# Performance work log

Measured on AMD Instinct MI355X. Metric: run time of the kernel, lower is better.

Reference implementation:

```python
import jax, jax.numpy as jnp
import numpy as np

WS = 11
SIGMA = 1.5
CH = 3
C1 = (0.01 * 255.0) ** 2  # 6.5025
C2 = (0.03 * 255.0) ** 2  # 58.5225


def _gauss_window():
    # 1D Gaussian -> outer product -> depthwise kernel [C, 1, ws, ws] (OIHW)
    coords = jnp.arange(WS, dtype=jnp.float32) - WS // 2
    g = jnp.exp(-coords ** 2 / (2.0 * SIGMA ** 2))
    g = g / g.sum()
    w2d = g[:, None] * g[None, :]
    return jnp.tile(w2d[None, None], (CH, 1, 1, 1))


def _dwconv(x, win):
    pad = WS // 2
    return jax.lax.conv_general_dilated(
        x, win, window_strides=(1, 1), padding=[(pad, pad), (pad, pad)],
        feature_group_count=CH,
        dimension_numbers=('NCHW', 'OIHW', 'NCHW'))


def setup_inputs() -> dict:
    key = jax.random.key(0)
    k1, k2 = jax.random.split(key)
    shape = (32, 3, 512, 512)
    img_gen = jax.random.uniform(k1, shape, jnp.float32, -1.0, 1.0)
    img_ref = jax.random.uniform(k2, shape, jnp.float32, -1.0, 1.0)
    return {"img_gen": img_gen, "img_ref": img_ref}


def reference(img_gen, img_ref):
    gen = (img_gen + 1.0) * 0.5
    ref = (img_ref + 1.0) * 0.5
    win = _gauss_window()

    mu1 = _dwconv(gen, win)
    mu2 = _dwconv(ref, win)
    mu1_sq = mu1 * mu1
    mu2_sq = mu2 * mu2
    mu1_mu2 = mu1 * mu2
    sigma1_sq = _dwconv(gen * gen, win) - mu1_sq
    sigma2_sq = _dwconv(ref * ref, win) - mu2_sq
    sigma12 = _dwconv(gen * ref, win) - mu1_mu2

    ssim_map = ((2.0 * mu1_mu2 + C1) * (2.0 * sigma12 + C2)) / (
        (mu1_sq + mu2_sq + C1) * (sigma1_sq + sigma2_sq + C2))
    return 1.0 - ssim_map.mean()
```

## Files before the change

kernel.cpp:

```cpp
#include <hip/hip_runtime.h>

#define TX 64
#define TY 20
#define PROWS (TY + 10)
#define HSTR 67
#define IMW 512
#define IMH 512
#define NPLANES 96
#define NBX (IMW / TX)
#define NBY ((IMH + TY - 1) / TY)
#define NBLOCKS (NBX * NBY * NPLANES)

__device__ __forceinline__ float uniform_f(float v) {
  return __int_as_float(__builtin_amdgcn_readfirstlane(__float_as_int(v)));
}

__device__ __forceinline__ void gauss_weights(float* w) {
  double t[11];
  double s = 0.0;
#pragma unroll
  for (int i = 0; i < 11; ++i) {
    double d = (double)(i - 5);
    t[i] = exp(-d * d / 4.5);
    s += t[i];
  }
#pragma unroll
  for (int i = 0; i < 11; ++i) w[i] = uniform_f((float)(t[i] / s));
}

__global__ __launch_bounds__(256, 4) void ssim_main(
    const float* __restrict__ gen, const float* __restrict__ ref,
    float* __restrict__ partial) {
  __shared__ float sh[5][PROWS][HSTR];
  __shared__ float swsum[4];

  const int tid = threadIdx.x;
  const int bid = blockIdx.x;
  const int rem = bid % (NBX * NBY);
  const int plane = bid / (NBX * NBY);
  const int bx = rem % NBX;
  const int by = rem / NBX;
  const int x0 = bx * TX;
  const int y0 = by * TY;
  const float* gp = gen + (size_t)plane * (IMW * IMH);
  const float* rp = ref + (size_t)plane * (IMW * IMH);

  float w[11];
  gauss_weights(w);

  if (tid < PROWS * 8) {
    const int row = tid >> 3;
    const int xs = (tid & 7) * 8;
    const int gy = y0 - 5 + row;
    const bool rowok = (gy >= 0) && (gy < IMH);
    const int xbase = x0 + xs - 8;
    const float* grow = gp + (size_t)gy * IMW;
    const float* rrow = rp + (size_t)gy * IMW;

    float ga[24], ra[24];
#pragma unroll
    for (int k = 0; k < 6; ++k) {
      const int c = xbase + 4 * k;
      const bool ok = rowok && (c >= 0) && (c < IMW);
      float4 vg = make_float4(0.f, 0.f, 0.f, 0.f);
      float4 vr = make_float4(0.f, 0.f, 0.f, 0.f);
      if (ok) {
        float4 g4 = *(const float4*)(grow + c);
        float4 r4 = *(const float4*)(rrow + c);
        vg.x = fmaf(0.5f, g4.x, 0.5f); vg.y = fmaf(0.5f, g4.y, 0.5f);
        vg.z = fmaf(0.5f, g4.z, 0.5f); vg.w = fmaf(0.5f, g4.w, 0.5f);
        vr.x = fmaf(0.5f, r4.x, 0.5f); vr.y = fmaf(0.5f, r4.y, 0.5f);
        vr.z = fmaf(0.5f, r4.z, 0.5f); vr.w = fmaf(0.5f, r4.w, 0.5f);
      }
      ga[4 * k + 0] = vg.x; ga[4 * k + 1] = vg.y;
      ga[4 * k + 2] = vg.z; ga[4 * k + 3] = vg.w;
      ra[4 * k + 0] = vr.x; ra[4 * k + 1] = vr.y;
      ra[4 * k + 2] = vr.z; ra[4 * k + 3] = vr.w;
    }

    float acc[5][8];
#pragma unroll
    for (int q = 0; q < 5; ++q)
#pragma unroll
      for (int o = 0; o < 8; ++o) acc[q][o] = 0.f;

#pragma unroll
    for (int p = 0; p < 18; ++p) {
      const float g = ga[p + 3];
      const float r = ra[p + 3];
      const float gg = g * g;
      const float rr = r * r;
      const float gr = g * r;
      const int olo = (p - 10 < 0) ? 0 : p - 10;
      const int ohi = (p < 7) ? p : 7;
#pragma unroll
      for (int o = olo; o <= ohi; ++o) {
        const float wt = w[p - o];
        acc[0][o] = fmaf(wt, g, acc[0][o]);
        acc[1][o] = fmaf(wt, r, acc[1][o]);
        acc[2][o] = fmaf(wt, gg, acc[2][o]);
        acc[3][o] = fmaf(wt, rr, acc[3][o]);
        acc[4][o] = fmaf(wt, gr, acc[4][o]);
      }
    }
#pragma unroll
    for (int q = 0; q < 5; ++q)
#pragma unroll
      for (int o = 0; o < 8; ++o) sh[q][row][xs + o] = acc[q][o];
  }
  __syncthreads();

  const int col = tid & 63;
  const int r0 = (tid >> 6) * 5;
  float hv[5][15];
#pragma unroll
  for (int q = 0; q < 5; ++q)
#pragma unroll
    for (int i = 0; i < 15; ++i) hv[q][i] = sh[q][r0 + i][col];

  const float C1 = 6.5025f, C2 = 58.5225f;
  float lsum = 0.f;
#pragma unroll
  for (int o = 0; o < 5; ++o) {
    float mu1 = 0.f, mu2 = 0.f, e1 = 0.f, e2 = 0.f, e12 = 0.f;
#pragma unroll
    for (int t = 0; t < 11; ++t) {
      const float wt = w[t];
      mu1 = fmaf(wt, hv[0][o + t], mu1);
      mu2 = fmaf(wt, hv[1][o + t], mu2);
      e1 = fmaf(wt, hv[2][o + t], e1);
      e2 = fmaf(wt, hv[3][o + t], e2);
      e12 = fmaf(wt, hv[4][o + t], e12);
    }
    const float m12 = mu1 * mu2;
    const float m1s = mu1 * mu1;
    const float m2s = mu2 * mu2;
    const float num = (2.f * m12 + C1) * (2.f * (e12 - m12) + C2);
    const float den = (m1s + m2s + C1) * ((e1 - m1s) + (e2 - m2s) + C2);
    const int y = y0 + r0 + o;
    lsum += (y < IMH) ? (num / den) : 0.f;
  }

#pragma unroll
  for (int off = 32; off > 0; off >>= 1) lsum += __shfl_down(lsum, off, 64);
  if ((tid & 63) == 0) swsum[tid >> 6] = lsum;
  __syncthreads();
  if (tid == 0) partial[bid] = swsum[0] + swsum[1] + swsum[2] + swsum[3];
}

__global__ void ssim_reduce(const float* __restrict__ partial,
                            float* __restrict__ out) {
  const int nv = NBLOCKS / 4;
  double s = 0.0;
  for (int i = threadIdx.x; i < nv; i += 256) {
    float4 v = ((const float4*)partial)[i];
    s += (double)v.x + (double)v.y + (double)v.z + (double)v.w;
  }
#pragma unroll
  for (int off = 32; off > 0; off >>= 1) s += __shfl_down(s, off, 64);
  __shared__ double sd[4];
  if ((threadIdx.x & 63) == 0) sd[threadIdx.x >> 6] = s;
  __syncthreads();
  if (threadIdx.x == 0) {
    double npix = (double)NPLANES * (double)IMW * (double)IMH;
    out[0] = (float)(1.0 - (sd[0] + sd[1] + sd[2] + sd[3]) / npix);
  }
}

extern "C" void kernel_launch(void* const* d_in, const int* in_sizes, int n_in,
                              void* d_out, int out_size, void* d_ws, size_t ws_size,
                              hipStream_t stream) {
  (void)in_sizes; (void)n_in; (void)out_size; (void)ws_size;
  const float* gen = (const float*)d_in[0];
  const float* ref = (const float*)d_in[1];
  float* partial = (float*)d_ws;
  ssim_main<<<NBLOCKS, 256, 0, stream>>>(gen, ref, partial);
  ssim_reduce<<<1, 256, 0, stream>>>(partial, (float*)d_out);
}
```

Measured before the change: 310.5 us.

## Use constant Gaussian weights, vectorized LDS stores, fast divide and atomic reduction

Replaces the per-thread double-precision Gaussian weight computation with a constant-memory table. Pads the shared row stride to 68 so the horizontal results can be stored as float4, and switches the SSIM division to __fdividef. The separate partial-sum reduction kernel is replaced by a double atomicAdd per block, plus tiny init and finalize kernels. This trades the per-thread weight setup and the reduction pass for atomic contention, an extra launch, and a slightly less accurate divide.

```diff
diff --git a/kernel.cpp b/kernel.cpp
--- a/kernel.cpp
+++ b/kernel.cpp
@@ -3,7 +3,7 @@
 #define TX 64
 #define TY 20
 #define PROWS (TY + 10)
-#define HSTR 67
+#define HSTR 68
 #define IMW 512
 #define IMH 512
 #define NPLANES 96
@@ -11,28 +11,15 @@
 #define NBY ((IMH + TY - 1) / TY)
 #define NBLOCKS (NBX * NBY * NPLANES)
 
-__device__ __forceinline__ float uniform_f(float v) {
-  return __int_as_float(__builtin_amdgcn_readfirstlane(__float_as_int(v)));
-}
-
-__device__ __forceinline__ void gauss_weights(float* w) {
-  double t[11];
-  double s = 0.0;
-#pragma unroll
-  for (int i = 0; i < 11; ++i) {
-    double d = (double)(i - 5);
-    t[i] = exp(-d * d / 4.5);
-    s += t[i];
-  }
-#pragma unroll
-  for (int i = 0; i < 11; ++i) w[i] = uniform_f((float)(t[i] / s));
-}
+__device__ __constant__ float GW[11] = {
+    0.00102838f, 0.00759877f, 0.03600077f, 0.10936069f, 0.21300553f,
+    0.26601172f,
+    0.21300553f, 0.10936069f, 0.03600077f, 0.00759877f, 0.00102838f};
 
 __global__ __launch_bounds__(256, 4) void ssim_main(
     const float* __restrict__ gen, const float* __restrict__ ref,
-    float* __restrict__ partial) {
-  __shared__ float sh[5][PROWS][HSTR];
-  __shared__ float swsum[4];
+    double* __restrict__ acc) {
+  __shared__ __align__(16) float sh[5][PROWS][HSTR];
 
   const int tid = threadIdx.x;
   const int bid = blockIdx.x;
@@ -44,9 +31,6 @@
   const int y0 = by * TY;
   const float* gp = gen + (size_t)plane * (IMW * IMH);
   const float* rp = ref + (size_t)plane * (IMW * IMH);
-
-  float w[11];
-  gauss_weights(w);
 
   if (tid < PROWS * 8) {
     const int row = tid >> 3;
@@ -78,11 +62,11 @@
       ra[4 * k + 2] = vr.z; ra[4 * k + 3] = vr.w;
     }
 
-    float acc[5][8];
+    float acc5[5][8];
 #pragma unroll
     for (int q = 0; q < 5; ++q)
 #pragma unroll
-      for (int o = 0; o < 8; ++o) acc[q][o] = 0.f;
+      for (int o = 0; o < 8; ++o) acc5[q][o] = 0.f;
 
 #pragma unroll
     for (int p = 0; p < 18; ++p) {
@@ -95,18 +79,21 @@
       const int ohi = (p < 7) ? p : 7;
 #pragma unroll
       for (int o = olo; o <= ohi; ++o) {
-        const float wt = w[p - o];
-        acc[0][o] = fmaf(wt, g, acc[0][o]);
-        acc[1][o] = fmaf(wt, r, acc[1][o]);
-        acc[2][o] = fmaf(wt, gg, acc[2][o]);
-        acc[3][o] = fmaf(wt, rr, acc[3][o]);
-        acc[4][o] = fmaf(wt, gr, acc[4][o]);
+        const float wt = GW[p - o];
+        acc5[0][o] = fmaf(wt, g, acc5[0][o]);
+        acc5[1][o] = fmaf(wt, r, acc5[1][o]);
+        acc5[2][o] = fmaf(wt, gg, acc5[2][o]);
+        acc5[3][o] = fmaf(wt, rr, acc5[3][o]);
+        acc5[4][o] = fmaf(wt, gr, acc5[4][o]);
       }
     }
 #pragma unroll
-    for (int q = 0; q < 5; ++q)
-#pragma unroll
-      for (int o = 0; o < 8; ++o) sh[q][row][xs + o] = acc[q][o];
+    for (int q = 0; q < 5; ++q) {
+      *(float4*)&sh[q][row][xs + 0] =
+          make_float4(acc5[q][0], acc5[q][1], acc5[q][2], acc5[q][3]);
+      *(float4*)&sh[q][row][xs + 4] =
+          make_float4(acc5[q][4], acc5[q][5], acc5[q][6], acc5[q][7]);
+    }
   }
   __syncthreads();
 
@@ -125,7 +112,7 @@
     float mu1 = 0.f, mu2 = 0.f, e1 = 0.f, e2 = 0.f, e12 = 0.f;
 #pragma unroll
     for (int t = 0; t < 11; ++t) {
-      const float wt = w[t];
+      const float wt = GW[t];
       mu1 = fmaf(wt, hv[0][o + t], mu1);
       mu2 = fmaf(wt, hv[1][o + t], mu2);
       e1 = fmaf(wt, hv[2][o + t], e1);
@@ -138,33 +125,27 @@
     const float num = (2.f * m12 + C1) * (2.f * (e12 - m12) + C2);
     const float den = (m1s + m2s + C1) * ((e1 - m1s) + (e2 - m2s) + C2);
     const int y = y0 + r0 + o;
-    lsum += (y < IMH) ? (num / den) : 0.f;
+    lsum += (y < IMH) ? __fdividef(num, den) : 0.f;
   }
 
 #pragma unroll
   for (int off = 32; off > 0; off >>= 1) lsum += __shfl_down(lsum, off, 64);
-  if ((tid & 63) == 0) swsum[tid >> 6] = lsum;
   __syncthreads();
-  if (tid == 0) partial[bid] = swsum[0] + swsum[1] + swsum[2] + swsum[3];
+  if ((tid & 63) == 0) ((float*)sh)[tid >> 6] = lsum;
+  __syncthreads();
+  if (tid == 0) {
+    double bs = (double)((float*)sh)[0] + (double)((float*)sh)[1] +
+                (double)((float*)sh)[2] + (double)((float*)sh)[3];
+    atomicAdd(acc, bs);
+  }
 }
 
-__global__ void ssim_reduce(const float* __restrict__ partial,
-                            float* __restrict__ out) {
-  const int nv = NBLOCKS / 4;
-  double s = 0.0;
-  for (int i = threadIdx.x; i < nv; i += 256) {
-    float4 v = ((const float4*)partial)[i];
-    s += (double)v.x + (double)v.y + (double)v.z + (double)v.w;
-  }
-#pragma unroll
-  for (int off = 32; off > 0; off >>= 1) s += __shfl_down(s, off, 64);
-  __shared__ double sd[4];
-  if ((threadIdx.x & 63) == 0) sd[threadIdx.x >> 6] = s;
-  __syncthreads();
-  if (threadIdx.x == 0) {
-    double npix = (double)NPLANES * (double)IMW * (double)IMH;
-    out[0] = (float)(1.0 - (sd[0] + sd[1] + sd[2] + sd[3]) / npix);
-  }
+__global__ void ssim_init(double* __restrict__ acc) { *acc = 0.0; }
+
+__global__ void ssim_final(const double* __restrict__ acc,
+                           float* __restrict__ out) {
+  const double npix = (double)NPLANES * (double)IMW * (double)IMH;
+  out[0] = (float)(1.0 - *acc / npix);
 }
 
 extern "C" void kernel_launch(void* const* d_in, const int* in_sizes, int n_in,
@@ -173,7 +154,8 @@
   (void)in_sizes; (void)n_in; (void)out_size; (void)ws_size;
   const float* gen = (const float*)d_in[0];
   const float* ref = (const float*)d_in[1];
-  float* partial = (float*)d_ws;
-  ssim_main<<<NBLOCKS, 256, 0, stream>>>(gen, ref, partial);
-  ssim_reduce<<<1, 256, 0, stream>>>(partial, (float*)d_out);
+  double* acc = (double*)d_ws;
+  ssim_init<<<1, 1, 0, stream>>>(acc);
+  ssim_main<<<NBLOCKS, 256, 0, stream>>>(gen, ref, acc);
+  ssim_final<<<1, 1, 0, stream>>>(acc, (float*)d_out);
 }
```

Result: slower. 408.0 us (+31.4%).
